# Optimization experiments

Hardware: AMD Instinct MI355X
Metric: run time of the kernel (lower is better)

## Reference

```python
import jax, jax.numpy as jnp
import numpy as np

M_CODES = 512
D_EMB = 128
COMMITMENT = 0.25
DECAY = 0.999
EPS = 1e-05


def setup_inputs() -> dict:
    key = jax.random.key(0)
    k1, k2, k3 = jax.random.split(key, 3)
    B, T = 32, 2048
    init_bound = 1.0 / M_CODES
    embedding = jax.random.uniform(k2, (M_CODES, D_EMB), jnp.float32, -init_bound, init_bound)
    return {
        'x': jax.random.normal(k1, (B, T, D_EMB), jnp.float32),
        'x_mask': jnp.ones((B, 1, T), jnp.float32),
        'embedding': embedding,
        'ema_count': jnp.zeros((M_CODES,), jnp.float32),
        'ema_weight': embedding,  # clone of embedding at init
    }


def reference(x, x_mask, embedding, ema_count, ema_weight):
    mask = jnp.transpose(x_mask, (0, 2, 1))  # [B, T, 1]
    xm = x * mask                            # masked input (named `x` in torch code)
    M, D = embedding.shape
    x_flat = jax.lax.stop_gradient(xm).reshape(-1, D)  # [N, D], N = B*T
    distances = (jnp.sum(embedding ** 2, axis=1)[None, :]
                 + jnp.sum(x_flat ** 2, axis=1, keepdims=True)
                 - 2.0 * (x_flat @ embedding.T))  # [N, M]
    indices = jnp.argmin(distances.astype(jnp.float32), axis=-1)  # [N]
    quantized = embedding[indices].reshape(xm.shape)  # gather + view_as(x)
    # --- EMA codebook update (training branch) ---
    # sum of one-hot encodings over tokens == per-code counts
    counts = jax.ops.segment_sum(jnp.ones_like(x_flat[:, 0]), indices, num_segments=M)
    new_count = DECAY * ema_count + (1.0 - DECAY) * counts
    n = jnp.sum(new_count)
    new_count = (new_count + EPS) / (n + M * EPS) * n
    # encodings.T @ x_flat == scatter-add of token features per code
    dw = jax.ops.segment_sum(x_flat, indices, num_segments=M)  # [M, D]
    new_weight = DECAY * ema_weight + (1.0 - DECAY) * dw
    new_embedding = new_weight / new_count[:, None]
    # --- commitment loss (quantized detached) ---
    e_latent_loss = jnp.sum((xm * mask - jax.lax.stop_gradient(quantized) * mask) ** 2) / (jnp.sum(mask) * x.shape[-1])
    loss = COMMITMENT * e_latent_loss
    # straight-through estimator
    q_st = (xm + jax.lax.stop_gradient(quantized - xm)) * mask
    return (q_st, loss, new_embedding, new_count, new_weight)
```

## Files before the change

kernel.cpp:

```cpp
#include <hip/hip_runtime.h>

#define M_CODES 512
#define D_EMB 128
#define D4 32
#define MARGIN 5e-5f
#define SCHUNK 1024

typedef short bf16x8 __attribute__((ext_vector_type(8)));
typedef float f32x4 __attribute__((ext_vector_type(4)));

__device__ __forceinline__ unsigned short f2bf(float f) {
    unsigned u = __float_as_uint(f);
    u += 0x7fffu + ((u >> 16) & 1u);
    return (unsigned short)(u >> 16);
}
__device__ __forceinline__ float bf2f(unsigned short h) {
    return __uint_as_float(((unsigned)h) << 16);
}

__device__ __forceinline__ float np_pairwise_sumsq128(const float* __restrict__ a,
                                                      float scale) {
    float r[8];
#pragma unroll
    for (int j = 0; j < 8; ++j) {
        float v = __fmul_rn(a[j], scale);
        r[j] = __fmul_rn(v, v);
    }
    for (int i = 8; i < 128; i += 8) {
#pragma unroll
        for (int j = 0; j < 8; ++j) {
            float v = __fmul_rn(a[i + j], scale);
            r[j] = __fadd_rn(r[j], __fmul_rn(v, v));
        }
    }
    return __fadd_rn(__fadd_rn(__fadd_rn(r[0], r[1]), __fadd_rn(r[2], r[3])),
                     __fadd_rn(__fadd_rn(r[4], r[5]), __fadd_rn(r[6], r[7])));
}

__global__ __launch_bounds__(256) void kSZ(const float* __restrict__ emb,
                                           float* __restrict__ sumE,
                                           float* __restrict__ embT,
                                           unsigned short* __restrict__ ebh,
                                           unsigned short* __restrict__ ebl,
                                           float* __restrict__ accc,
                                           int* __restrict__ flagCnt) {
    int tid = threadIdx.x, wid = tid >> 6, lane = tid & 63;
    int m = blockIdx.x * 4 + wid;
    int gi = blockIdx.x * 256 + tid;
    if (gi < M_CODES) accc[gi] = 0.f;
    if (gi == 0) *flagCnt = 0;
    const float* er = emb + (size_t)m * D_EMB;
    float r = 0.f;
    if (lane < 8) {
        float v = __fmul_rn(er[lane], 1.0f);
        r = __fmul_rn(v, v);
        for (int i = 1; i < 16; ++i) {
            float w = __fmul_rn(er[8 * i + lane], 1.0f);
            r = __fadd_rn(r, __fmul_rn(w, w));
        }
    }
    float s1 = __fadd_rn(r, __shfl_xor(r, 1, 64));
    float s2 = __fadd_rn(s1, __shfl_xor(s1, 2, 64));
    float s3 = __fadd_rn(s2, __shfl_xor(s2, 4, 64));
    if (lane == 0) sumE[m] = s3;
#pragma unroll
    for (int dd = lane; dd < D_EMB; dd += 64) {
        float e = er[dd];
        embT[dd * M_CODES + m] = e;
        unsigned short hh = f2bf(e);
        ebh[(size_t)m * D_EMB + dd] = hh;
        ebl[(size_t)m * D_EMB + dd] = f2bf(e - bf2f(hh));
    }
}

__global__ __launch_bounds__(256) void kA(const float* __restrict__ x,
                                          const float* __restrict__ xmask,
                                          const unsigned short* __restrict__ ebh,
                                          const unsigned short* __restrict__ ebl,
                                          const float* __restrict__ sumE,
                                          int* __restrict__ idx_out,
                                          int* __restrict__ flagCnt,
                                          int* __restrict__ flagList,
                                          float* __restrict__ lossW,
                                          float* __restrict__ maskW, int N) {
    __shared__ unsigned short hb[2][4096];
    __shared__ unsigned short lb[2][4096];
    __shared__ float xnS[4][32], mkS[4][32];
    int tid = threadIdx.x;
    int wid = tid >> 6, lane = tid & 63;
    int m = lane & 15, kg = lane >> 4;
    int tok0 = blockIdx.x * 128 + wid * 32;

    bf16x8 ah0[4], al0[4], ah1[4], al1[4];
    float xn0 = 0.f, xn1 = 0.f;
    float mk0 = xmask[tok0 + m], mk1 = xmask[tok0 + 16 + m];
#pragma unroll
    for (int ks = 0; ks < 4; ++ks) {
        const float4* p0 = reinterpret_cast<const float4*>(
            x + (size_t)(tok0 + m) * D_EMB + ks * 32 + kg * 8);
        const float4* p1 = reinterpret_cast<const float4*>(
            x + (size_t)(tok0 + 16 + m) * D_EMB + ks * 32 + kg * 8);
        float4 a0 = p0[0], a1 = p0[1], c0 = p1[0], c1 = p1[1];
        float e0[8] = {a0.x, a0.y, a0.z, a0.w, a1.x, a1.y, a1.z, a1.w};
        float e1[8] = {c0.x, c0.y, c0.z, c0.w, c1.x, c1.y, c1.z, c1.w};
        bf16x8 h0, l0, h1, l1;
#pragma unroll
        for (int j = 0; j < 8; ++j) {
            float v0 = e0[j] * mk0;
            xn0 = fmaf(v0, v0, xn0);
            unsigned short hh0 = f2bf(v0);
            h0[j] = (short)hh0;
            l0[j] = (short)f2bf(v0 - bf2f(hh0));
            float v1 = e1[j] * mk1;
            xn1 = fmaf(v1, v1, xn1);
            unsigned short hh1 = f2bf(v1);
            h1[j] = (short)hh1;
            l1[j] = (short)f2bf(v1 - bf2f(hh1));
        }
        ah0[ks] = h0; al0[ks] = l0; ah1[ks] = h1; al1[ks] = l1;
    }
    xn0 += __shfl_xor(xn0, 16, 64);
    xn0 += __shfl_xor(xn0, 32, 64);
    xn1 += __shfl_xor(xn1, 16, 64);
    xn1 += __shfl_xor(xn1, 32, 64);
    if (kg == 0) {
        xnS[wid][m] = xn0; mkS[wid][m] = mk0;
        xnS[wid][16 + m] = xn1; mkS[wid][16 + m] = mk1;
    }

    float b1[2][4], b2[2][4];
    int bi[2][4];
#pragma unroll
    for (int tt = 0; tt < 2; ++tt)
#pragma unroll
        for (int r = 0; r < 4; ++r) {
            b1[tt][r] = 3.4e38f; b2[tt][r] = 3.4e38f; bi[tt][r] = 0x7fffffff;
        }

    int mo = tid >> 4, sl = tid & 15;
    int dstIdx = mo * 128 + (sl >> 3) * 64 + ((sl & 7) ^ (mo & 7)) * 8;
    float4 sh0, sv0, sh1, sv1;
#define LOADREGS(t)                                                            \
    {                                                                          \
        sh0 = *reinterpret_cast<const float4*>(                                \
            ebh + (size_t)((t) * 32 + mo) * D_EMB + sl * 8);                   \
        sv0 = *reinterpret_cast<const float4*>(                                \
            ebl + (size_t)((t) * 32 + mo) * D_EMB + sl * 8);                   \
        sh1 = *reinterpret_cast<const float4*>(                                \
            ebh + (size_t)((t) * 32 + 16 + mo) * D_EMB + sl * 8);              \
        sv1 = *reinterpret_cast<const float4*>(                                \
            ebl + (size_t)((t) * 32 + 16 + mo) * D_EMB + sl * 8);              \
    }
#define WRITEB(b)                                                              \
    {                                                                          \
        *reinterpret_cast<float4*>(&hb[b][dstIdx]) = sh0;                      \
        *reinterpret_cast<float4*>(&lb[b][dstIdx]) = sv0;                      \
        *reinterpret_cast<float4*>(&hb[b][2048 + dstIdx]) = sh1;               \
        *reinterpret_cast<float4*>(&lb[b][2048 + dstIdx]) = sv1;               \
    }

    LOADREGS(0);
    WRITEB(0);
    __syncthreads();
    for (int t = 0; t < 16; ++t) {
        int cur = t & 1;
        if (t < 15) LOADREGS(t + 1);
#pragma unroll
        for (int sub = 0; sub < 2; ++sub) {
            bf16x8 bh[4], bl[4];
#pragma unroll
            for (int ks = 0; ks < 4; ++ks) {
                int off = sub * 2048 + m * 128 + (ks >> 1) * 64 +
                          ((((ks & 1) * 4 + kg)) ^ (m & 7)) * 8;
                bh[ks] = *reinterpret_cast<const bf16x8*>(&hb[cur][off]);
                bl[ks] = *reinterpret_cast<const bf16x8*>(&lb[cur][off]);
            }
            f32x4 accA0 = {0.f, 0.f, 0.f, 0.f}, accB0 = {0.f, 0.f, 0.f, 0.f};
            f32x4 accA1 = {0.f, 0.f, 0.f, 0.f}, accB1 = {0.f, 0.f, 0.f, 0.f};
#pragma unroll
            for (int ks = 0; ks < 2; ++ks) {
                accA0 = __builtin_amdgcn_mfma_f32_16x16x32_bf16(ah0[ks], bh[ks], accA0, 0, 0, 0);
                accA0 = __builtin_amdgcn_mfma_f32_16x16x32_bf16(al0[ks], bh[ks], accA0, 0, 0, 0);
                accA0 = __builtin_amdgcn_mfma_f32_16x16x32_bf16(ah0[ks], bl[ks], accA0, 0, 0, 0);
                accA1 = __builtin_amdgcn_mfma_f32_16x16x32_bf16(ah1[ks], bh[ks], accA1, 0, 0, 0);
                accA1 = __builtin_amdgcn_mfma_f32_16x16x32_bf16(al1[ks], bh[ks], accA1, 0, 0, 0);
                accA1 = __builtin_amdgcn_mfma_f32_16x16x32_bf16(ah1[ks], bl[ks], accA1, 0, 0, 0);
            }
#pragma unroll
            for (int ks = 2; ks < 4; ++ks) {
                accB0 = __builtin_amdgcn_mfma_f32_16x16x32_bf16(ah0[ks], bh[ks], accB0, 0, 0, 0);
                accB0 = __builtin_amdgcn_mfma_f32_16x16x32_bf16(al0[ks], bh[ks], accB0, 0, 0, 0);
                accB0 = __builtin_amdgcn_mfma_f32_16x16x32_bf16(ah0[ks], bl[ks], accB0, 0, 0, 0);
                accB1 = __builtin_amdgcn_mfma_f32_16x16x32_bf16(ah1[ks], bh[ks], accB1, 0, 0, 0);
                accB1 = __builtin_amdgcn_mfma_f32_16x16x32_bf16(al1[ks], bh[ks], accB1, 0, 0, 0);
                accB1 = __builtin_amdgcn_mfma_f32_16x16x32_bf16(ah1[ks], bl[ks], accB1, 0, 0, 0);
            }
            int c = t * 32 + sub * 16 + m;
            float sE = sumE[c];
#pragma unroll
            for (int r = 0; r < 4; ++r) {
                float s0 = fmaf(-2.f, accA0[r] + accB0[r], sE);
                if (s0 < b1[0][r]) { b2[0][r] = b1[0][r]; b1[0][r] = s0; bi[0][r] = c; }
                else if (s0 < b2[0][r]) b2[0][r] = s0;
                float s1 = fmaf(-2.f, accA1[r] + accB1[r], sE);
                if (s1 < b1[1][r]) { b2[1][r] = b1[1][r]; b1[1][r] = s1; bi[1][r] = c; }
                else if (s1 < b2[1][r]) b2[1][r] = s1;
            }
        }
        if (t < 15) WRITEB(cur ^ 1);
        __syncthreads();
    }
#undef LOADREGS
#undef WRITEB
#pragma unroll
    for (int off = 1; off <= 8; off <<= 1) {
#pragma unroll
        for (int tt = 0; tt < 2; ++tt)
#pragma unroll
            for (int r = 0; r < 4; ++r) {
                float o1 = __shfl_xor(b1[tt][r], off, 64);
                float o2 = __shfl_xor(b2[tt][r], off, 64);
                int oi = __shfl_xor(bi[tt][r], off, 64);
                if (o1 < b1[tt][r] || (o1 == b1[tt][r] && oi < bi[tt][r])) {
                    b2[tt][r] = fminf(b1[tt][r], o2); b1[tt][r] = o1; bi[tt][r] = oi;
                } else {
                    b2[tt][r] = fminf(b2[tt][r], o1);
                }
            }
    }
    float liS = 0.f, mkT = 0.f;
#pragma unroll
    for (int tt = 0; tt < 2; ++tt)
#pragma unroll
        for (int r = 0; r < 4; ++r) {
            int row = kg * 4 + r;
            float mkr = mkS[wid][tt * 16 + row], xnr = xnS[wid][tt * 16 + row];
            liS += mkr * mkr * (xnr + b1[tt][r]);
            mkT += mkr;
            if (m == 0) {
                int tokr = tok0 + tt * 16 + row;
                idx_out[tokr] = bi[tt][r];
                if (b2[tt][r] - b1[tt][r] < MARGIN) {
                    int pp = atomicAdd(flagCnt, 1);
                    flagList[pp] = tokr;
                }
            }
        }
    liS += __shfl_xor(liS, 16, 64);
    liS += __shfl_xor(liS, 32, 64);
    mkT += __shfl_xor(mkT, 16, 64);
    mkT += __shfl_xor(mkT, 32, 64);
    if (lane == 0) {
        int grp = blockIdx.x * 4 + wid;
        lossW[grp] = liS;
        maskW[grp] = mkT;
    }
}

__global__ __launch_bounds__(256) void kF(const float* __restrict__ x,
                                          const float* __restrict__ xmask,
                                          const float* __restrict__ embT,
                                          const float* __restrict__ sumE,
                                          const int* __restrict__ flagCnt,
                                          const int* __restrict__ flagList,
                                          int* __restrict__ idx_out) {
    int wave = (blockIdx.x * 256 + threadIdx.x) >> 6;
    int lane = threadIdx.x & 63;
    int nW = gridDim.x * 4;
    int cnt = *flagCnt;
    for (int j = wave; j < cnt; j += nW) {
        int t = flagList[j];
        float mk = xmask[t];
        const float* xr = x + (size_t)t * D_EMB;
        float sx = np_pairwise_sumsq128(xr, mk);
        float acc[8];
#pragma unroll
        for (int cb = 0; cb < 8; ++cb) acc[cb] = 0.f;
        for (int i = 0; i < D_EMB; ++i) {
            float xi = __fmul_rn(xr[i], mk);
#pragma unroll
            for (int cb = 0; cb < 8; ++cb)
                acc[cb] = __fmaf_rn(xi, embT[i * M_CODES + cb * 64 + lane], acc[cb]);
        }
        float best = 3.4e38f;
        int bq = 0x7fffffff;
#pragma unroll
        for (int cb = 0; cb < 8; ++cb) {
            int c = cb * 64 + lane;
            float d = __fsub_rn(__fadd_rn(sumE[c], sx), __fmul_rn(2.f, acc[cb]));
            if (d < best || (d == best && c < bq)) { best = d; bq = c; }
        }
#pragma unroll
        for (int off = 32; off > 0; off >>= 1) {
            float s2 = __shfl_xor(best, off, 64);
            int i2 = __shfl_xor(bq, off, 64);
            if (s2 < best || (s2 == best && i2 < bq)) { best = s2; bq = i2; }
        }
        if (lane == 0) idx_out[t] = bq;
    }
}

__global__ __launch_bounds__(256) void kScat(const float* __restrict__ x,
                                             const float* __restrict__ emb,
                                             const float* __restrict__ xmask,
                                             const int* __restrict__ idx,
                                             float* __restrict__ q_st,
                                             float* __restrict__ partialD,
                                             float* __restrict__ accc,
                                             int N, int nch) {
    __shared__ float accD[16 * M_CODES];
    __shared__ float accC[M_CODES];
    int bid = blockIdx.x;
    int q = bid / nch, ch = bid - q * nch;
    int tid = threadIdx.x;
    for (int i = tid; i < 16 * M_CODES; i += 256) accD[i] = 0.f;
    if (q == 0)
        for (int i = tid; i < M_CODES; i += 256) accC[i] = 0.f;
    __syncthreads();
    int tl = tid >> 1, dl = tid & 1;
    int base = ch * SCHUNK;
    for (int it = 0; it < SCHUNK / 128; ++it) {
        int t = base + it * 128 + tl;
        if (t < N) {
            int id = idx[t];
            float mk = xmask[t];
            const float4* xp = reinterpret_cast<const float4*>(
                x + (size_t)t * D_EMB + q * 16 + dl * 8);
            const float4* ep = reinterpret_cast<const float4*>(
                emb + (size_t)id * D_EMB + q * 16 + dl * 8);
            float4 xv0 = xp[0], xv1 = xp[1];
            float4 ev0 = ep[0], ev1 = ep[1];
            float4 o0, o1;
            o0.x = ev0.x * mk; o0.y = ev0.y * mk; o0.z = ev0.z * mk; o0.w = ev0.w * mk;
            o1.x = ev1.x * mk; o1.y = ev1.y * mk; o1.z = ev1.z * mk; o1.w = ev1.w * mk;
            float4* qp = reinterpret_cast<float4*>(
                q_st + (size_t)t * D_EMB + q * 16 + dl * 8);
            qp[0] = o0; qp[1] = o1;
            float vx[8] = {xv0.x * mk, xv0.y * mk, xv0.z * mk, xv0.w * mk,
                           xv1.x * mk, xv1.y * mk, xv1.z * mk, xv1.w * mk};
            int d0 = dl * 8;
#pragma unroll
            for (int j = 0; j < 8; ++j)
                atomicAdd(&accD[(d0 + j) * M_CODES + id], vx[j]);
            if (q == 0 && dl == 0) atomicAdd(&accC[id], 1.f);
        }
    }
    __syncthreads();
    float* pD = partialD + (size_t)bid * (16 * M_CODES);
    for (int i = tid; i < 16 * M_CODES; i += 256) pD[i] = accD[i];
    if (q == 0)
        for (int i = tid; i < M_CODES; i += 256) atomicAdd(&accc[i], accC[i]);
}

__global__ __launch_bounds__(256) void kWD2(const float* __restrict__ partialD,
                                            const float* __restrict__ ema_w,
                                            const float* __restrict__ counts,
                                            const float* __restrict__ ema_count,
                                            const float* __restrict__ lossP,
                                            const float* __restrict__ maskP,
                                            float* __restrict__ new_w,
                                            float* __restrict__ new_emb,
                                            float* __restrict__ new_cnt,
                                            float* __restrict__ loss_out,
                                            int nch, int nP) {
    __shared__ float red[256];
    int tid = threadIdx.x;
    float part = 0.999f * ema_count[tid] + 0.001f * counts[tid];
    part += 0.999f * ema_count[tid + 256] + 0.001f * counts[tid + 256];
    red[tid] = part;
    __syncthreads();
#pragma unroll
    for (int s = 128; s > 0; s >>= 1) {
        if (tid < s) red[tid] += red[tid + s];
        __syncthreads();
    }
    float nsum = red[0];
    __syncthreads();

    int i = blockIdx.x * 256 + tid;
    int c = i & 511;
    int d = i >> 9;
    int q = d >> 4, dd = d & 15;
    float raw = 0.999f * ema_count[c] + 0.001f * counts[c];
    float norm = (raw + 1e-5f) / (nsum + (float)M_CODES * 1e-5f) * nsum;
    float s = 0.f;
    for (int ch = 0; ch < nch; ++ch)
        s += partialD[(size_t)(q * nch + ch) * (16 * M_CODES) + dd * M_CODES + c];
    size_t o = (size_t)c * D_EMB + d;
    float w = 0.999f * ema_w[o] + 0.001f * s;
    new_w[o] = w;
    new_emb[o] = w / norm;
    if (d == 0) new_cnt[c] = norm;

    if (blockIdx.x == 0) {
        float lp = 0.f, mp = 0.f;
        for (int j = tid; j < nP; j += 256) { lp += lossP[j]; mp += maskP[j]; }
        red[tid] = lp;
        __syncthreads();
#pragma unroll
        for (int ss = 128; ss > 0; ss >>= 1) {
            if (tid < ss) red[tid] += red[tid + ss];
            __syncthreads();
        }
        float S = red[0];
        __syncthreads();
        red[tid] = mp;
        __syncthreads();
#pragma unroll
        for (int ss = 128; ss > 0; ss >>= 1) {
            if (tid < ss) red[tid] += red[tid + ss];
            __syncthreads();
        }
        if (tid == 0) loss_out[0] = 0.25f * S / (red[0] * (float)D_EMB);
    }
}

extern "C" void kernel_launch(void* const* d_in, const int* in_sizes, int n_in,
                              void* d_out, int out_size, void* d_ws, size_t ws_size,
                              hipStream_t stream) {
    const float* x = (const float*)d_in[0];
    const float* xmask = (const float*)d_in[1];
    const float* emb = (const float*)d_in[2];
    const float* ema_count = (const float*)d_in[3];
    const float* ema_weight = (const float*)d_in[4];
    int N = in_sizes[0] / D_EMB;

    float* out = (float*)d_out;
    float* q_st = out;
    float* loss = out + (size_t)N * D_EMB;
    float* new_emb = loss + 1;
    float* new_cnt = new_emb + M_CODES * D_EMB;
    float* new_w = new_cnt + M_CODES;

    int nGrp = N / 32;
    int nch = (N + SCHUNK - 1) / SCHUNK;
    float* fws = (float*)d_ws;
    int* idx = (int*)fws;
    float* counts = fws + N;
    float* norm = counts + M_CODES;
    float* lossP = norm + M_CODES;
    float* maskP = lossP + nGrp;
    float* sumE = maskP + nGrp;
    int* flagCnt = (int*)(sumE + M_CODES);
    int* flagList = flagCnt + 4;
    float* embT = (float*)(flagList + N);
    unsigned short* ebh = (unsigned short*)(embT + M_CODES * D_EMB);
    unsigned short* ebl = ebh + M_CODES * D_EMB;
    float* partialD = (float*)(ebl + M_CODES * D_EMB);

    hipLaunchKernelGGL(kSZ, dim3(128), dim3(256), 0, stream,
                       emb, sumE, embT, ebh, ebl, counts, flagCnt);
    hipLaunchKernelGGL(kA, dim3(N / 128), dim3(256), 0, stream, x, xmask, ebh,
                       ebl, sumE, idx, flagCnt, flagList, lossP, maskP, N);
    hipLaunchKernelGGL(kF, dim3(1024), dim3(256), 0, stream, x, xmask, embT, sumE,
                       flagCnt, flagList, idx);
    hipLaunchKernelGGL(kScat, dim3(8 * nch), dim3(256), 0, stream, x, emb, xmask,
                       idx, q_st, partialD, counts, N, nch);
    hipLaunchKernelGGL(kWD2, dim3(M_CODES * D_EMB / 256), dim3(256), 0, stream,
                       partialD, ema_weight, counts, ema_count, lossP, maskP,
                       new_w, new_emb, new_cnt, loss, nch, nGrp);
}
```

Baseline: 133.7 us.

## Split quantized output write into separate kernel and widen scatter blocks

Moves the gather and write of the quantized output into a new fully coalesced kernel, one float4 per thread, and removes it from the scatter kernel. The scatter kernel now uses 512 threads, with each thread handling 4 dims instead of 8 for the shared-memory atomic accumulation. The aim is better coalescing on the q_st write and more parallelism in the atomic phase. In exchange it adds a kernel launch and an extra read of idx and mask, and the scatter block now has more threads contending on the shared atomics.

```diff
diff --git a/kernel.cpp b/kernel.cpp
--- a/kernel.cpp
+++ b/kernel.cpp
@@ -300,11 +300,26 @@
     }
 }
 
-__global__ __launch_bounds__(256) void kScat(const float* __restrict__ x,
-                                             const float* __restrict__ emb,
+__global__ __launch_bounds__(256) void kQ(const float* __restrict__ emb,
+                                          const float* __restrict__ xmask,
+                                          const int* __restrict__ idx,
+                                          float* __restrict__ q_st, int N) {
+    int g = blockIdx.x * 256 + threadIdx.x;
+    int t = g >> 5;
+    int d4 = g & 31;
+    if (t < N) {
+        int id = idx[t];
+        float mk = xmask[t];
+        float4 ev = reinterpret_cast<const float4*>(emb)[(size_t)id * D4 + d4];
+        float4 o;
+        o.x = ev.x * mk; o.y = ev.y * mk; o.z = ev.z * mk; o.w = ev.w * mk;
+        reinterpret_cast<float4*>(q_st)[(size_t)t * D4 + d4] = o;
+    }
+}
+
+__global__ __launch_bounds__(512) void kScat(const float* __restrict__ x,
                                              const float* __restrict__ xmask,
                                              const int* __restrict__ idx,
-                                             float* __restrict__ q_st,
                                              float* __restrict__ partialD,
                                              float* __restrict__ accc,
                                              int N, int nch) {
@@ -313,43 +328,32 @@
     int bid = blockIdx.x;
     int q = bid / nch, ch = bid - q * nch;
     int tid = threadIdx.x;
-    for (int i = tid; i < 16 * M_CODES; i += 256) accD[i] = 0.f;
+    for (int i = tid; i < 16 * M_CODES; i += 512) accD[i] = 0.f;
     if (q == 0)
-        for (int i = tid; i < M_CODES; i += 256) accC[i] = 0.f;
+        for (int i = tid; i < M_CODES; i += 512) accC[i] = 0.f;
     __syncthreads();
-    int tl = tid >> 1, dl = tid & 1;
+    int tl = tid >> 2, dl = tid & 3;
     int base = ch * SCHUNK;
     for (int it = 0; it < SCHUNK / 128; ++it) {
         int t = base + it * 128 + tl;
         if (t < N) {
             int id = idx[t];
             float mk = xmask[t];
-            const float4* xp = reinterpret_cast<const float4*>(
-                x + (size_t)t * D_EMB + q * 16 + dl * 8);
-            const float4* ep = reinterpret_cast<const float4*>(
-                emb + (size_t)id * D_EMB + q * 16 + dl * 8);
-            float4 xv0 = xp[0], xv1 = xp[1];
-            float4 ev0 = ep[0], ev1 = ep[1];
-            float4 o0, o1;
-            o0.x = ev0.x * mk; o0.y = ev0.y * mk; o0.z = ev0.z * mk; o0.w = ev0.w * mk;
-            o1.x = ev1.x * mk; o1.y = ev1.y * mk; o1.z = ev1.z * mk; o1.w = ev1.w * mk;
-            float4* qp = reinterpret_cast<float4*>(
-                q_st + (size_t)t * D_EMB + q * 16 + dl * 8);
-            qp[0] = o0; qp[1] = o1;
-            float vx[8] = {xv0.x * mk, xv0.y * mk, xv0.z * mk, xv0.w * mk,
-                           xv1.x * mk, xv1.y * mk, xv1.z * mk, xv1.w * mk};
-            int d0 = dl * 8;
-#pragma unroll
-            for (int j = 0; j < 8; ++j)
-                atomicAdd(&accD[(d0 + j) * M_CODES + id], vx[j]);
+            float4 xv = *reinterpret_cast<const float4*>(
+                x + (size_t)t * D_EMB + q * 16 + dl * 4);
+            int d0 = dl * 4;
+            atomicAdd(&accD[(d0 + 0) * M_CODES + id], xv.x * mk);
+            atomicAdd(&accD[(d0 + 1) * M_CODES + id], xv.y * mk);
+            atomicAdd(&accD[(d0 + 2) * M_CODES + id], xv.z * mk);
+            atomicAdd(&accD[(d0 + 3) * M_CODES + id], xv.w * mk);
             if (q == 0 && dl == 0) atomicAdd(&accC[id], 1.f);
         }
     }
     __syncthreads();
     float* pD = partialD + (size_t)bid * (16 * M_CODES);
-    for (int i = tid; i < 16 * M_CODES; i += 256) pD[i] = accD[i];
+    for (int i = tid; i < 16 * M_CODES; i += 512) pD[i] = accD[i];
     if (q == 0)
-        for (int i = tid; i < M_CODES; i += 256) atomicAdd(&accc[i], accC[i]);
+        for (int i = tid; i < M_CODES; i += 512) atomicAdd(&accc[i], accC[i]);
 }
 
 __global__ __launch_bounds__(256) void kWD2(const float* __restrict__ partialD,
@@ -454,8 +458,10 @@
                        ebl, sumE, idx, flagCnt, flagList, lossP, maskP, N);
     hipLaunchKernelGGL(kF, dim3(1024), dim3(256), 0, stream, x, xmask, embT, sumE,
                        flagCnt, flagList, idx);
-    hipLaunchKernelGGL(kScat, dim3(8 * nch), dim3(256), 0, stream, x, emb, xmask,
-                       idx, q_st, partialD, counts, N, nch);
+    hipLaunchKernelGGL(kQ, dim3((N * 32 + 255) / 256), dim3(256), 0, stream,
+                       emb, xmask, idx, q_st, N);
+    hipLaunchKernelGGL(kScat, dim3(8 * nch), dim3(512), 0, stream, x, xmask,
+                       idx, partialD, counts, N, nch);
     hipLaunchKernelGGL(kWD2, dim3(M_CODES * D_EMB / 256), dim3(256), 0, stream,
                        partialD, ema_weight, counts, ema_count, lossP, maskP,
                        new_w, new_emb, new_cnt, loss, nch, nGrp);
```

Result: slower. 142.1 us (+6.2%).

## Restructure scatter kernel to 1024-thread blocks with 32-dim slices and padded LDS

Applied to the files above, without the earlier changes.

The scatter/EMA accumulation kernel now runs 1024-thread blocks that each own 32 embedding dimensions instead of 16, so half as many blocks are launched. Each block stages its chunk's indices and mask in shared memory first. Each thread handles one float4 per token, so a warp reads contiguous 128B rows of x. The per-dimension shared accumulator rows are padded to stride 513 to spread atomics across banks. Larger LDS use (about 70KB) limits occupancy, and the partial-sum layout and the reduce kernel are changed to match. The kernel also now assumes N is a multiple of the chunk size, since the bounds check was removed.

```diff
diff --git a/kernel.cpp b/kernel.cpp
--- a/kernel.cpp
+++ b/kernel.cpp
@@ -5,6 +5,7 @@
 #define D4 32
 #define MARGIN 5e-5f
 #define SCHUNK 1024
+#define ADSTRIDE 513
 
 typedef short bf16x8 __attribute__((ext_vector_type(8)));
 typedef float f32x4 __attribute__((ext_vector_type(4)));
@@ -300,56 +301,54 @@
     }
 }
 
-__global__ __launch_bounds__(256) void kScat(const float* __restrict__ x,
-                                             const float* __restrict__ emb,
-                                             const float* __restrict__ xmask,
-                                             const int* __restrict__ idx,
-                                             float* __restrict__ q_st,
-                                             float* __restrict__ partialD,
-                                             float* __restrict__ accc,
-                                             int N, int nch) {
-    __shared__ float accD[16 * M_CODES];
+__global__ __launch_bounds__(1024) void kScat(const float* __restrict__ x,
+                                              const float* __restrict__ emb,
+                                              const float* __restrict__ xmask,
+                                              const int* __restrict__ idx,
+                                              float* __restrict__ q_st,
+                                              float* __restrict__ partialD,
+                                              float* __restrict__ accc,
+                                              int N, int nch) {
+    __shared__ float accD[32 * ADSTRIDE];
+    __shared__ int idxL[SCHUNK];
+    __shared__ float mkL[SCHUNK];
     __shared__ float accC[M_CODES];
     int bid = blockIdx.x;
     int q = bid / nch, ch = bid - q * nch;
     int tid = threadIdx.x;
-    for (int i = tid; i < 16 * M_CODES; i += 256) accD[i] = 0.f;
+    for (int i = tid; i < 32 * ADSTRIDE; i += 1024) accD[i] = 0.f;
     if (q == 0)
-        for (int i = tid; i < M_CODES; i += 256) accC[i] = 0.f;
+        for (int i = tid; i < M_CODES; i += 1024) accC[i] = 0.f;
+    int base = ch * SCHUNK;
+    idxL[tid] = idx[base + tid];
+    mkL[tid] = xmask[base + tid];
     __syncthreads();
-    int tl = tid >> 1, dl = tid & 1;
-    int base = ch * SCHUNK;
+    if (q == 0) atomicAdd(&accC[idxL[tid]], 1.f);
+    int tl = tid >> 3, dl = tid & 7;
     for (int it = 0; it < SCHUNK / 128; ++it) {
-        int t = base + it * 128 + tl;
-        if (t < N) {
-            int id = idx[t];
-            float mk = xmask[t];
-            const float4* xp = reinterpret_cast<const float4*>(
-                x + (size_t)t * D_EMB + q * 16 + dl * 8);
-            const float4* ep = reinterpret_cast<const float4*>(
-                emb + (size_t)id * D_EMB + q * 16 + dl * 8);
-            float4 xv0 = xp[0], xv1 = xp[1];
-            float4 ev0 = ep[0], ev1 = ep[1];
-            float4 o0, o1;
-            o0.x = ev0.x * mk; o0.y = ev0.y * mk; o0.z = ev0.z * mk; o0.w = ev0.w * mk;
-            o1.x = ev1.x * mk; o1.y = ev1.y * mk; o1.z = ev1.z * mk; o1.w = ev1.w * mk;
-            float4* qp = reinterpret_cast<float4*>(
-                q_st + (size_t)t * D_EMB + q * 16 + dl * 8);
-            qp[0] = o0; qp[1] = o1;
-            float vx[8] = {xv0.x * mk, xv0.y * mk, xv0.z * mk, xv0.w * mk,
-                           xv1.x * mk, xv1.y * mk, xv1.z * mk, xv1.w * mk};
-            int d0 = dl * 8;
-#pragma unroll
-            for (int j = 0; j < 8; ++j)
-                atomicAdd(&accD[(d0 + j) * M_CODES + id], vx[j]);
-            if (q == 0 && dl == 0) atomicAdd(&accC[id], 1.f);
-        }
+        int t = it * 128 + tl;
+        int id = idxL[t];
+        float mk = mkL[t];
+        size_t fo = (size_t)(base + t) * D4 + q * 8 + dl;
+        float4 xv = reinterpret_cast<const float4*>(x)[fo];
+        float4 ev = reinterpret_cast<const float4*>(emb)[(size_t)id * D4 + q * 8 + dl];
+        float4 o;
+        o.x = ev.x * mk; o.y = ev.y * mk; o.z = ev.z * mk; o.w = ev.w * mk;
+        reinterpret_cast<float4*>(q_st)[fo] = o;
+        int d0 = dl * 4;
+        atomicAdd(&accD[(d0 + 0) * ADSTRIDE + id], xv.x * mk);
+        atomicAdd(&accD[(d0 + 1) * ADSTRIDE + id], xv.y * mk);
+        atomicAdd(&accD[(d0 + 2) * ADSTRIDE + id], xv.z * mk);
+        atomicAdd(&accD[(d0 + 3) * ADSTRIDE + id], xv.w * mk);
     }
     __syncthreads();
-    float* pD = partialD + (size_t)bid * (16 * M_CODES);
-    for (int i = tid; i < 16 * M_CODES; i += 256) pD[i] = accD[i];
+    float* pD = partialD + (size_t)bid * (32 * M_CODES);
+    for (int i = tid; i < 32 * M_CODES; i += 1024) {
+        int dd = i >> 9, c = i & 511;
+        pD[i] = accD[dd * ADSTRIDE + c];
+    }
     if (q == 0)
-        for (int i = tid; i < M_CODES; i += 256) atomicAdd(&accc[i], accC[i]);
+        for (int i = tid; i < M_CODES; i += 1024) atomicAdd(&accc[i], accC[i]);
 }
 
 __global__ __launch_bounds__(256) void kWD2(const float* __restrict__ partialD,
@@ -380,12 +379,12 @@
     int i = blockIdx.x * 256 + tid;
     int c = i & 511;
     int d = i >> 9;
-    int q = d >> 4, dd = d & 15;
+    int q = d >> 5, dd = d & 31;
     float raw = 0.999f * ema_count[c] + 0.001f * counts[c];
     float norm = (raw + 1e-5f) / (nsum + (float)M_CODES * 1e-5f) * nsum;
     float s = 0.f;
     for (int ch = 0; ch < nch; ++ch)
-        s += partialD[(size_t)(q * nch + ch) * (16 * M_CODES) + dd * M_CODES + c];
+        s += partialD[(size_t)(q * nch + ch) * (32 * M_CODES) + dd * M_CODES + c];
     size_t o = (size_t)c * D_EMB + d;
     float w = 0.999f * ema_w[o] + 0.001f * s;
     new_w[o] = w;
@@ -454,8 +453,8 @@
                        ebl, sumE, idx, flagCnt, flagList, lossP, maskP, N);
     hipLaunchKernelGGL(kF, dim3(1024), dim3(256), 0, stream, x, xmask, embT, sumE,
                        flagCnt, flagList, idx);
-    hipLaunchKernelGGL(kScat, dim3(8 * nch), dim3(256), 0, stream, x, emb, xmask,
-                       idx, q_st, partialD, counts, N, nch);
+    hipLaunchKernelGGL(kScat, dim3(4 * nch), dim3(1024), 0, stream, x, emb,
+                       xmask, idx, q_st, partialD, counts, N, nch);
     hipLaunchKernelGGL(kWD2, dim3(M_CODES * D_EMB / 256), dim3(256), 0, stream,
                        partialD, ema_weight, counts, ema_count, lossP, maskP,
                        new_w, new_emb, new_cnt, loss, nch, nGrp);
```

After: 135.2 us. About the same (+1.1%).
